# Performance work log

Hardware: AMD Instinct MI355X
Metric: run time of the kernel (lower is better)

## Reference

```python
import jax, jax.numpy as jnp
import numpy as np

D = 512          # model_dim
H = 4 * D        # hidden_mult * model_dim
E = 8            # n_experts
TEMP = 1.0       # temperature
EPS = 1e-5       # torch LayerNorm eps


def setup_inputs() -> dict:
    key = jax.random.key(0)
    ks = jax.random.split(key, 6)
    x = jax.random.normal(ks[0], (4, 4096, D), dtype=jnp.float32)
    # gate: LayerNorm(D) + Linear(D, E)
    gate_gamma = jnp.ones((D,), jnp.float32)
    gate_beta = jnp.zeros((D,), jnp.float32)
    gate_W = jax.random.normal(ks[1], (D, E), jnp.float32) * 0.02
    gate_b = jnp.zeros((E,), jnp.float32)
    # experts stacked along leading E axis: Linear(D,H) -> LeakyReLU -> Linear(H,D)
    W1 = jax.random.normal(ks[2], (E, D, H), jnp.float32) * 0.02
    b1 = jnp.zeros((E, H), jnp.float32)
    W2 = jax.random.normal(ks[3], (E, H, D), jnp.float32) * 0.02
    b2 = jnp.zeros((E, D), jnp.float32)
    return {"x": x, "gate_gamma": gate_gamma, "gate_beta": gate_beta,
            "gate_W": gate_W, "gate_b": gate_b,
            "W1": W1, "b1": b1, "W2": W2, "b2": b2}


def reference(x, gate_gamma, gate_beta, gate_W, gate_b, W1, b1, W2, b2):
    # gate: LayerNorm then Linear, temperature-scaled softmax
    mu = jnp.mean(x, axis=-1, keepdims=True)
    var = jnp.var(x, axis=-1, keepdims=True)  # biased, as in torch LayerNorm
    xn = (x - mu) * jax.lax.rsqrt(var + EPS) * gate_gamma + gate_beta
    logits = (xn @ gate_W + gate_b) / TEMP          # [B,N,E]
    w = jax.nn.softmax(logits, axis=-1)             # [B,N,E]
    # run every expert on all tokens (faithful to soft routing)
    h = jnp.einsum('bnd,edh->benh', x, W1) + b1[None, :, None, :]  # [B,E,N,H]
    h = jax.nn.leaky_relu(h, negative_slope=0.01)
    y = jnp.einsum('benh,ehd->bend', h, W2) + b2[None, :, None, :]  # [B,E,N,D]
    # gate-weighted combine over experts
    out = jnp.einsum('bend,bne->bnd', y, w)
    return out
```

## Files before the change

### kernel.cpp

```cpp
#include <hip/hip_runtime.h>
#include <stdint.h>

#define TD 512
#define TH 2048
#define TE 8
#define TT 16384

typedef __bf16 bf16x8 __attribute__((ext_vector_type(8)));
typedef __bf16 bf16x4 __attribute__((ext_vector_type(4)));
typedef float  f32x4  __attribute__((ext_vector_type(4)));

__device__ __forceinline__ void async16(const void* src, void* lds) {
    __builtin_amdgcn_global_load_lds((const __attribute__((address_space(1))) uint32_t*)src,
                                     (__attribute__((address_space(3))) uint32_t*)lds,
                                     16, 0, 0);
}

__global__ __launch_bounds__(256) void gate_kernel(
    const float* __restrict__ x, const float* __restrict__ gamma,
    const float* __restrict__ beta, const float* __restrict__ gW,
    const float* __restrict__ gb, const float* __restrict__ b2,
    float* __restrict__ gate_w, __bf16* __restrict__ xb,
    float* __restrict__ outp)
{
    const int t    = blockIdx.x * 4 + (threadIdx.x >> 6);
    const int lane = threadIdx.x & 63;

    const float* xr = x + (size_t)t * TD + lane * 8;
    float4 v0 = *(const float4*)xr;
    float4 v1 = *(const float4*)(xr + 4);
    float xv[8] = {v0.x, v0.y, v0.z, v0.w, v1.x, v1.y, v1.z, v1.w};

    float s = 0.f, sq = 0.f;
    #pragma unroll
    for (int j = 0; j < 8; ++j) { s += xv[j]; sq += xv[j] * xv[j]; }
    #pragma unroll
    for (int off = 32; off > 0; off >>= 1) {
        s  += __shfl_xor(s, off);
        sq += __shfl_xor(sq, off);
    }
    const float mean = s * (1.f / TD);
    const float var  = sq * (1.f / TD) - mean * mean;
    const float rs   = rsqrtf(var + 1e-5f);

    bf16x8 xc;
    #pragma unroll
    for (int j = 0; j < 8; ++j) xc[j] = (__bf16)xv[j];
    *(bf16x8*)&xb[(size_t)t * TD + lane * 8] = xc;

    float p[TE] = {};
    #pragma unroll
    for (int j = 0; j < 8; ++j) {
        const int d = lane * 8 + j;
        const float xn = (xv[j] - mean) * rs * gamma[d] + beta[d];
        const float* wr = gW + (size_t)d * TE;
        #pragma unroll
        for (int e = 0; e < TE; ++e) p[e] += xn * wr[e];
    }
    #pragma unroll
    for (int off = 32; off > 0; off >>= 1) {
        #pragma unroll
        for (int e = 0; e < TE; ++e) p[e] += __shfl_xor(p[e], off);
    }

    float m = -3.4e38f;
    #pragma unroll
    for (int e = 0; e < TE; ++e) { p[e] += gb[e]; m = fmaxf(m, p[e]); }
    float sum = 0.f;
    #pragma unroll
    for (int e = 0; e < TE; ++e) { p[e] = expf(p[e] - m); sum += p[e]; }
    const float inv = 1.f / sum;
    if (lane == 0) {
        #pragma unroll
        for (int e = 0; e < TE; ++e) gate_w[(size_t)t * TE + e] = p[e] * inv;
    }

    float ob[8] = {};
    #pragma unroll
    for (int e = 0; e < TE; ++e) {
        const float we = p[e] * inv;
        const float* b2r = b2 + (size_t)e * TD + lane * 8;
        #pragma unroll
        for (int j = 0; j < 8; ++j) ob[j] += we * b2r[j];
    }
    float4 o0 = {ob[0], ob[1], ob[2], ob[3]};
    float4 o1 = {ob[4], ob[5], ob[6], ob[7]};
    *(float4*)&outp[(size_t)t * TD + lane * 8]     = o0;
    *(float4*)&outp[(size_t)t * TD + lane * 8 + 4] = o1;
}

template <int MODE>
__global__ __launch_bounds__(256) void tcast(
    const float* __restrict__ src, __bf16* __restrict__ dst, int R, int C)
{
    __shared__ __bf16 tile[64][65];
    const int e  = blockIdx.z;
    const int r0 = blockIdx.y * 64, c0 = blockIdx.x * 64;
    const int tr = threadIdx.x >> 6;
    const int tc = threadIdx.x & 63;

    const float* s = src + ((size_t)e * R + r0) * C + c0;
    #pragma unroll
    for (int i = 0; i < 16; ++i) {
        const int r = i * 4 + tr;
        tile[r][tc] = (__bf16)s[(size_t)r * C + tc];
    }
    __syncthreads();

    size_t RS, eoff;
    if (MODE == 0) { RS = (size_t)R;     eoff = (size_t)e * C * R; }
    else           { RS = (size_t)2 * R; eoff = (size_t)(e >> 1) * C * 2 * R + (size_t)(e & 1) * R; }

    __bf16* d = dst + eoff + (size_t)c0 * RS + r0;
    #pragma unroll
    for (int i = 0; i < 16; ++i) {
        const int c = i * 4 + tr;
        d[(size_t)c * RS + tc] = tile[tc][c];
    }
}

__global__ __launch_bounds__(256, 2) void gemm1m(
    const __bf16* __restrict__ A, const __bf16* __restrict__ Bt,
    const float* __restrict__ b1, const float* __restrict__ gw,
    __bf16* __restrict__ hC, int grp)
{
    constexpr int S  = TD;
    constexpr int NG = 64;

    __shared__ __align__(16) char smem[49152];

    const int tid  = threadIdx.x;
    const int w    = tid >> 6, lane = tid & 63;
    const int fr   = lane & 15, ks = lane >> 4;

    const int bmg = blockIdx.x & 31;
    const int r   = blockIdx.x >> 5;
    const int bn  = r & 7;
    const int e2  = r >> 3;
    const int e   = grp * 2 + e2;

    const __bf16* Ab  = A  + (size_t)bmg * 512 * S;
    const __bf16* Bb  = Bt + (size_t)e2 * TH * TD + (size_t)bn * 256 * S;
    const float*  b1e = b1 + (size_t)e * TH;

    f32x4 acc[8][4] = {};

    auto stage = [&](int g, int b) {
        const int m4 = g >> 4, kt = g & 15;
        char* aRegion = smem + b * 8192;
        char* bRegion = smem + 16384 + b * 16384;
        const __bf16* Am = Ab + (size_t)m4 * 128 * S;
        #pragma unroll
        for (int p = 0; p < 2; ++p) {
            const int cid = p * 256 + tid;
            const int row = cid >> 2;
            const int gc  = (cid & 3) ^ ((row >> 1) & 3);
            async16(Am + (size_t)row * S + kt * 32 + gc * 8, aRegion + cid * 16);
        }
        #pragma unroll
        for (int p = 0; p < 4; ++p) {
            const int cid = p * 256 + tid;
            const int row = cid >> 2;
            const int gc  = (cid & 3) ^ ((row >> 1) & 3);
            async16(Bb + (size_t)row * S + kt * 32 + gc * 8, bRegion + cid * 16);
        }
    };

    stage(0, 0);
    stage(1, 1);

    for (int g = 0; g < NG; ++g) {
        const int buf = g & 1;
        const char* aR = smem + buf * 8192;
        const char* bR = smem + 16384 + buf * 16384;

        if (g + 1 < NG) { asm volatile("s_waitcnt vmcnt(6)" ::: "memory"); }
        else            { asm volatile("s_waitcnt vmcnt(0)" ::: "memory"); }
        __builtin_amdgcn_sched_barrier(0);
        __builtin_amdgcn_s_barrier();

        bf16x8 areg[8], breg[4];
        #pragma unroll
        for (int m = 0; m < 8; ++m) {
            const int row = m * 16 + fr;
            areg[m] = *(const bf16x8*)(aR + row * 64 + (((ks ^ (row >> 1)) & 3) << 4));
        }
        #pragma unroll
        for (int n = 0; n < 4; ++n) {
            const int row = w * 64 + n * 16 + fr;
            breg[n] = *(const bf16x8*)(bR + row * 64 + (((ks ^ (row >> 1)) & 3) << 4));
        }
        asm volatile("s_waitcnt lgkmcnt(0)" ::: "memory");
        __builtin_amdgcn_sched_barrier(0);
        __builtin_amdgcn_s_barrier();

        if (g + 2 < NG) stage(g + 2, buf);

        __builtin_amdgcn_s_setprio(1);
        #pragma unroll
        for (int m = 0; m < 8; ++m)
            #pragma unroll
            for (int n = 0; n < 4; ++n)
                acc[m][n] = __builtin_amdgcn_mfma_f32_16x16x32_bf16(breg[n], areg[m], acc[m][n], 0, 0, 0);
        __builtin_amdgcn_s_setprio(0);
        __builtin_amdgcn_sched_barrier(0);

        if ((g & 15) == 15) {
            const int m4  = g >> 4;
            const int rjc = (lane >> 4) << 2;
            #pragma unroll
            for (int m = 0; m < 8; ++m) {
                const int row = (bmg * 4 + m4) * 128 + m * 16 + fr;
                const float wgt = gw[(size_t)row * TE + e];
                __bf16* hrow = hC + (size_t)row * (2 * TH) + e2 * TH;
                #pragma unroll
                for (int n = 0; n < 4; ++n) {
                    const int colb = bn * 256 + w * 64 + n * 16 + rjc;
                    const f32x4 bv = *(const f32x4*)&b1e[colb];
                    bf16x4 ov;
                    #pragma unroll
                    for (int j = 0; j < 4; ++j) {
                        float v = acc[m][n][j] + bv[j];
                        v = v > 0.f ? v : 0.01f * v;
                        ov[j] = (__bf16)(v * wgt);
                        acc[m][n][j] = 0.f;
                    }
                    *(bf16x4*)&hrow[colb] = ov;
                }
            }
        }
    }
}

__global__ __launch_bounds__(256, 4) void gemm2f(
    const __bf16* __restrict__ A, const __bf16* __restrict__ Bt,
    float* __restrict__ oC)
{
    constexpr int S  = 2 * TH;
    constexpr int NT = 128;

    __shared__ __align__(16) char smem[32768];

    const int tid  = threadIdx.x;
    const int w    = tid >> 6, lane = tid & 63;
    const int wr   = w >> 1, wc = w & 1;
    const int fr   = lane & 15, ks = lane >> 4;

    const int bm = blockIdx.x & 127;
    const int bn = blockIdx.x >> 7;

    const __bf16* Ab = A  + (size_t)bm * 128 * S;
    const __bf16* Bb = Bt + (size_t)bn * 128 * S;

    f32x4 acc[4][4] = {};

    auto stage = [&](int t, int b) {
        char* aRegion = smem + b * 8192;
        char* bRegion = smem + 16384 + b * 8192;
        #pragma unroll
        for (int p = 0; p < 2; ++p) {
            const int cid = p * 256 + tid;
            const int row = cid >> 2;
            const int gc  = (cid & 3) ^ ((row >> 1) & 3);
            async16(Ab + (size_t)row * S + t * 32 + gc * 8, aRegion + cid * 16);
        }
        #pragma unroll
        for (int p = 0; p < 2; ++p) {
            const int cid = p * 256 + tid;
            const int row = cid >> 2;
            const int gc  = (cid & 3) ^ ((row >> 1) & 3);
            async16(Bb + (size_t)row * S + t * 32 + gc * 8, bRegion + cid * 16);
        }
    };

    stage(0, 0);
    stage(1, 1);

    for (int t = 0; t < NT; ++t) {
        const int buf = t & 1;
        const char* aR = smem + buf * 8192;
        const char* bR = smem + 16384 + buf * 8192;

        if (t + 1 < NT) { asm volatile("s_waitcnt vmcnt(4)" ::: "memory"); }
        else            { asm volatile("s_waitcnt vmcnt(0)" ::: "memory"); }
        __builtin_amdgcn_sched_barrier(0);
        __builtin_amdgcn_s_barrier();

        bf16x8 areg[4], breg[4];
        #pragma unroll
        for (int m = 0; m < 4; ++m) {
            const int row = wr * 64 + m * 16 + fr;
            areg[m] = *(const bf16x8*)(aR + row * 64 + (((ks ^ (row >> 1)) & 3) << 4));
        }
        #pragma unroll
        for (int n = 0; n < 4; ++n) {
            const int row = wc * 64 + n * 16 + fr;
            breg[n] = *(const bf16x8*)(bR + row * 64 + (((ks ^ (row >> 1)) & 3) << 4));
        }
        asm volatile("s_waitcnt lgkmcnt(0)" ::: "memory");
        __builtin_amdgcn_sched_barrier(0);
        __builtin_amdgcn_s_barrier();

        if (t + 2 < NT) stage(t + 2, buf);

        __builtin_amdgcn_s_setprio(1);
        #pragma unroll
        for (int m = 0; m < 4; ++m)
            #pragma unroll
            for (int n = 0; n < 4; ++n)
                acc[m][n] = __builtin_amdgcn_mfma_f32_16x16x32_bf16(areg[m], breg[n], acc[m][n], 0, 0, 0);
        __builtin_amdgcn_s_setprio(0);
        __builtin_amdgcn_sched_barrier(0);
    }

    const int rj = (lane >> 4) << 2;
    #pragma unroll
    for (int m = 0; m < 4; ++m) {
        const int gr0 = bm * 128 + wr * 64 + m * 16 + rj;
        #pragma unroll
        for (int j = 0; j < 4; ++j) {
            const int gr = gr0 + j;
            #pragma unroll
            for (int n = 0; n < 4; ++n) {
                const int gc = bn * 128 + wc * 64 + n * 16 + fr;
                float* op = oC + (size_t)gr * TD + gc;
                *op += acc[m][n][j];
            }
        }
    }
}

extern "C" void kernel_launch(void* const* d_in, const int* in_sizes, int n_in,
                              void* d_out, int out_size, void* d_ws, size_t ws_size,
                              hipStream_t stream)
{
    const float* x     = (const float*)d_in[0];
    const float* gamma = (const float*)d_in[1];
    const float* beta  = (const float*)d_in[2];
    const float* gW    = (const float*)d_in[3];
    const float* gb    = (const float*)d_in[4];
    const float* W1    = (const float*)d_in[5];
    const float* b1    = (const float*)d_in[6];
    const float* W2    = (const float*)d_in[7];
    const float* b2    = (const float*)d_in[8];

    char* ws = (char*)d_ws;
    size_t off = 0;
    float*  gate_w = (float*)(ws + off);  off += (size_t)TT * TE * 4;
    __bf16* xb     = (__bf16*)(ws + off); off += (size_t)TT * TD * 2;
    __bf16* W1t    = (__bf16*)(ws + off); off += (size_t)TE * TD * TH * 2;
    __bf16* W2tc   = (__bf16*)(ws + off); off += (size_t)TE * TD * TH * 2;
    __bf16* h      = (__bf16*)(ws + off);

    gate_kernel<<<TT / 4, 256, 0, stream>>>(x, gamma, beta, gW, gb, b2,
                                            gate_w, xb, (float*)d_out);
    tcast<0><<<dim3(TH / 64, TD / 64, TE), 256, 0, stream>>>(W1, W1t, TD, TH);
    tcast<1><<<dim3(TD / 64, TH / 64, TE), 256, 0, stream>>>(W2, W2tc, TH, TD);

    for (int grp = 0; grp < 4; ++grp) {
        gemm1m<<<512, 256, 0, stream>>>(
            xb, W1t + (size_t)grp * 2 * TH * TD, b1, gate_w, h, grp);
        gemm2f<<<512, 256, 0, stream>>>(
            h, W2tc + (size_t)grp * TD * 2 * TH, (float*)d_out);
    }
}
```

Baseline: 774.4 us.

## Software-pipeline expert GEMMs by fusing GEMM1 of expert c with GEMM2 of c-1

Replaces the four grouped gemm1/gemm2 launch pairs with nine launches of a single fused kernel. Each launch runs GEMM1 for expert c and GEMM2 for expert c-1 concurrently in different blocks, using double-buffered h0/h1 buffers so the two stages overlap and fill the GPU. It also removes the paired-expert W2 layout in favour of per-expert K=2048 GEMM2, and defers the next-stage prefetch until after the epilogue at tile boundaries. The cost is one extra h buffer, GEMM2 blocks running at the 2-blocks-per-CU launch bound instead of 4, and more launches.

```diff
diff --git a/kernel.cpp b/kernel.cpp
--- a/kernel.cpp
+++ b/kernel.cpp
@@ -89,7 +89,6 @@
     *(float4*)&outp[(size_t)t * TD + lane * 8 + 4] = o1;
 }
 
-template <int MODE>
 __global__ __launch_bounds__(256) void tcast(
     const float* __restrict__ src, __bf16* __restrict__ dst, int R, int C)
 {
@@ -107,224 +106,217 @@
     }
     __syncthreads();
 
-    size_t RS, eoff;
-    if (MODE == 0) { RS = (size_t)R;     eoff = (size_t)e * C * R; }
-    else           { RS = (size_t)2 * R; eoff = (size_t)(e >> 1) * C * 2 * R + (size_t)(e & 1) * R; }
-
-    __bf16* d = dst + eoff + (size_t)c0 * RS + r0;
+    __bf16* d = dst + (size_t)e * C * R + (size_t)c0 * R + r0;
     #pragma unroll
     for (int i = 0; i < 16; ++i) {
         const int c = i * 4 + tr;
-        d[(size_t)c * RS + tc] = tile[tc][c];
-    }
-}
-
-__global__ __launch_bounds__(256, 2) void gemm1m(
-    const __bf16* __restrict__ A, const __bf16* __restrict__ Bt,
+        d[(size_t)c * R + tc] = tile[tc][c];
+    }
+}
+
+__global__ __launch_bounds__(256, 2) void moe_fused(
+    const __bf16* __restrict__ xb, const __bf16* __restrict__ W1t,
     const float* __restrict__ b1, const float* __restrict__ gw,
-    __bf16* __restrict__ hC, int grp)
+    __bf16* __restrict__ h0, __bf16* __restrict__ h1,
+    const __bf16* __restrict__ W2t, float* __restrict__ oC,
+    int c, int g1n)
 {
-    constexpr int S  = TD;
-    constexpr int NG = 64;
-
     __shared__ __align__(16) char smem[49152];
 
     const int tid  = threadIdx.x;
     const int w    = tid >> 6, lane = tid & 63;
     const int fr   = lane & 15, ks = lane >> 4;
 
-    const int bmg = blockIdx.x & 31;
-    const int r   = blockIdx.x >> 5;
-    const int bn  = r & 7;
-    const int e2  = r >> 3;
-    const int e   = grp * 2 + e2;
-
-    const __bf16* Ab  = A  + (size_t)bmg * 512 * S;
-    const __bf16* Bb  = Bt + (size_t)e2 * TH * TD + (size_t)bn * 256 * S;
-    const float*  b1e = b1 + (size_t)e * TH;
-
-    f32x4 acc[8][4] = {};
-
-    auto stage = [&](int g, int b) {
-        const int m4 = g >> 4, kt = g & 15;
-        char* aRegion = smem + b * 8192;
-        char* bRegion = smem + 16384 + b * 16384;
-        const __bf16* Am = Ab + (size_t)m4 * 128 * S;
-        #pragma unroll
-        for (int p = 0; p < 2; ++p) {
-            const int cid = p * 256 + tid;
-            const int row = cid >> 2;
-            const int gc  = (cid & 3) ^ ((row >> 1) & 3);
-            async16(Am + (size_t)row * S + kt * 32 + gc * 8, aRegion + cid * 16);
+    if ((int)blockIdx.x < g1n) {
+        const int e = c;
+        __bf16* hD = (c & 1) ? h1 : h0;
+        const __bf16* W1e = W1t + (size_t)e * TH * TD;
+        const float*  b1e = b1 + (size_t)e * TH;
+
+        const int bmg = blockIdx.x & 31;
+        const int bn  = blockIdx.x >> 5;
+        const __bf16* Ab = xb  + (size_t)bmg * 512 * TD;
+        const __bf16* Bb = W1e + (size_t)bn * 256 * TD;
+
+        f32x4 acc[8][4] = {};
+        constexpr int NG = 64;
+
+        auto stage = [&](int g, int b) {
+            const int m4 = g >> 4, kt = g & 15;
+            char* aRegion = smem + b * 8192;
+            char* bRegion = smem + 16384 + b * 16384;
+            const __bf16* Am = Ab + (size_t)m4 * 128 * TD;
+            #pragma unroll
+            for (int p = 0; p < 2; ++p) {
+                const int cid = p * 256 + tid;
+                const int row = cid >> 2;
+                const int gc  = (cid & 3) ^ ((row >> 1) & 3);
+                async16(Am + (size_t)row * TD + kt * 32 + gc * 8, aRegion + cid * 16);
+            }
+            #pragma unroll
+            for (int p = 0; p < 4; ++p) {
+                const int cid = p * 256 + tid;
+                const int row = cid >> 2;
+                const int gc  = (cid & 3) ^ ((row >> 1) & 3);
+                async16(Bb + (size_t)row * TD + kt * 32 + gc * 8, bRegion + cid * 16);
+            }
+        };
+
+        stage(0, 0);
+        stage(1, 1);
+
+        for (int g = 0; g < NG; ++g) {
+            const int buf = g & 1;
+            const char* aR = smem + buf * 8192;
+            const char* bR = smem + 16384 + buf * 16384;
+            const bool bnd = (g & 15) == 15;
+
+            if (g + 1 < NG) { asm volatile("s_waitcnt vmcnt(6)" ::: "memory"); }
+            else            { asm volatile("s_waitcnt vmcnt(0)" ::: "memory"); }
+            __builtin_amdgcn_sched_barrier(0);
+            __builtin_amdgcn_s_barrier();
+
+            bf16x8 areg[8], breg[4];
+            #pragma unroll
+            for (int m = 0; m < 8; ++m) {
+                const int row = m * 16 + fr;
+                areg[m] = *(const bf16x8*)(aR + row * 64 + (((ks ^ (row >> 1)) & 3) << 4));
+            }
+            #pragma unroll
+            for (int n = 0; n < 4; ++n) {
+                const int row = w * 64 + n * 16 + fr;
+                breg[n] = *(const bf16x8*)(bR + row * 64 + (((ks ^ (row >> 1)) & 3) << 4));
+            }
+            asm volatile("s_waitcnt lgkmcnt(0)" ::: "memory");
+            __builtin_amdgcn_sched_barrier(0);
+            __builtin_amdgcn_s_barrier();
+
+            if (!bnd && g + 2 < NG) stage(g + 2, buf);
+
+            __builtin_amdgcn_s_setprio(1);
+            #pragma unroll
+            for (int m = 0; m < 8; ++m)
+                #pragma unroll
+                for (int n = 0; n < 4; ++n)
+                    acc[m][n] = __builtin_amdgcn_mfma_f32_16x16x32_bf16(breg[n], areg[m], acc[m][n], 0, 0, 0);
+            __builtin_amdgcn_s_setprio(0);
+            __builtin_amdgcn_sched_barrier(0);
+
+            if (bnd) {
+                const int m4  = g >> 4;
+                const int rjc = (lane >> 4) << 2;
+                #pragma unroll
+                for (int m = 0; m < 8; ++m) {
+                    const int row = (bmg * 4 + m4) * 128 + m * 16 + fr;
+                    const float wgt = gw[(size_t)row * TE + e];
+                    __bf16* hrow = hD + (size_t)row * TH;
+                    #pragma unroll
+                    for (int n = 0; n < 4; ++n) {
+                        const int colb = bn * 256 + w * 64 + n * 16 + rjc;
+                        const f32x4 bv = *(const f32x4*)&b1e[colb];
+                        bf16x4 ov;
+                        #pragma unroll
+                        for (int j = 0; j < 4; ++j) {
+                            float v = acc[m][n][j] + bv[j];
+                            v = v > 0.f ? v : 0.01f * v;
+                            ov[j] = (__bf16)(v * wgt);
+                            acc[m][n][j] = 0.f;
+                        }
+                        *(bf16x4*)&hrow[colb] = ov;
+                    }
+                }
+                if (g + 2 < NG) stage(g + 2, buf);
+            }
         }
-        #pragma unroll
-        for (int p = 0; p < 4; ++p) {
-            const int cid = p * 256 + tid;
-            const int row = cid >> 2;
-            const int gc  = (cid & 3) ^ ((row >> 1) & 3);
-            async16(Bb + (size_t)row * S + kt * 32 + gc * 8, bRegion + cid * 16);
+    } else {
+        const int e = c - 1;
+        const __bf16* hS  = (e & 1) ? h1 : h0;
+        const __bf16* W2e = W2t + (size_t)e * TD * TH;
+
+        const int bid2 = blockIdx.x - g1n;
+        const int bm   = bid2 & 127;
+        const int bn   = bid2 >> 7;
+        constexpr int S  = TH;
+        constexpr int NT = 64;
+
+        const int wr = w >> 1, wc = w & 1;
+        const __bf16* Ab = hS  + (size_t)bm * 128 * S;
+        const __bf16* Bb = W2e + (size_t)bn * 128 * S;
+
+        f32x4 acc[4][4] = {};
+
+        auto stage = [&](int t, int b) {
+            char* aRegion = smem + b * 8192;
+            char* bRegion = smem + 16384 + b * 8192;
+            #pragma unroll
+            for (int p = 0; p < 2; ++p) {
+                const int cid = p * 256 + tid;
+                const int row = cid >> 2;
+                const int gc  = (cid & 3) ^ ((row >> 1) & 3);
+                async16(Ab + (size_t)row * S + t * 32 + gc * 8, aRegion + cid * 16);
+            }
+            #pragma unroll
+            for (int p = 0; p < 2; ++p) {
+                const int cid = p * 256 + tid;
+                const int row = cid >> 2;
+                const int gc  = (cid & 3) ^ ((row >> 1) & 3);
+                async16(Bb + (size_t)row * S + t * 32 + gc * 8, bRegion + cid * 16);
+            }
+        };
+
+        stage(0, 0);
+        stage(1, 1);
+
+        for (int t = 0; t < NT; ++t) {
+            const int buf = t & 1;
+            const char* aR = smem + buf * 8192;
+            const char* bR = smem + 16384 + buf * 8192;
+
+            if (t + 1 < NT) { asm volatile("s_waitcnt vmcnt(4)" ::: "memory"); }
+            else            { asm volatile("s_waitcnt vmcnt(0)" ::: "memory"); }
+            __builtin_amdgcn_sched_barrier(0);
+            __builtin_amdgcn_s_barrier();
+
+            bf16x8 areg[4], breg[4];
+            #pragma unroll
+            for (int m = 0; m < 4; ++m) {
+                const int row = wr * 64 + m * 16 + fr;
+                areg[m] = *(const bf16x8*)(aR + row * 64 + (((ks ^ (row >> 1)) & 3) << 4));
+            }
+            #pragma unroll
+            for (int n = 0; n < 4; ++n) {
+                const int row = wc * 64 + n * 16 + fr;
+                breg[n] = *(const bf16x8*)(bR + row * 64 + (((ks ^ (row >> 1)) & 3) << 4));
+            }
+            asm volatile("s_waitcnt lgkmcnt(0)" ::: "memory");
+            __builtin_amdgcn_sched_barrier(0);
+            __builtin_amdgcn_s_barrier();
+
+            if (t + 2 < NT) stage(t + 2, buf);
+
+            __builtin_amdgcn_s_setprio(1);
+            #pragma unroll
+            for (int m = 0; m < 4; ++m)
+                #pragma unroll
+                for (int n = 0; n < 4; ++n)
+                    acc[m][n] = __builtin_amdgcn_mfma_f32_16x16x32_bf16(areg[m], breg[n], acc[m][n], 0, 0, 0);
+            __builtin_amdgcn_s_setprio(0);
+            __builtin_amdgcn_sched_barrier(0);
         }
-    };
-
-    stage(0, 0);
-    stage(1, 1);
-
-    for (int g = 0; g < NG; ++g) {
-        const int buf = g & 1;
-        const char* aR = smem + buf * 8192;
-        const char* bR = smem + 16384 + buf * 16384;
-
-        if (g + 1 < NG) { asm volatile("s_waitcnt vmcnt(6)" ::: "memory"); }
-        else            { asm volatile("s_waitcnt vmcnt(0)" ::: "memory"); }
-        __builtin_amdgcn_sched_barrier(0);
-        __builtin_amdgcn_s_barrier();
-
-        bf16x8 areg[8], breg[4];
-        #pragma unroll
-        for (int m = 0; m < 8; ++m) {
-            const int row = m * 16 + fr;
-            areg[m] = *(const bf16x8*)(aR + row * 64 + (((ks ^ (row >> 1)) & 3) << 4));
-        }
-        #pragma unroll
-        for (int n = 0; n < 4; ++n) {
-            const int row = w * 64 + n * 16 + fr;
-            breg[n] = *(const bf16x8*)(bR + row * 64 + (((ks ^ (row >> 1)) & 3) << 4));
-        }
-        asm volatile("s_waitcnt lgkmcnt(0)" ::: "memory");
-        __builtin_amdgcn_sched_barrier(0);
-        __builtin_amdgcn_s_barrier();
-
-        if (g + 2 < NG) stage(g + 2, buf);
-
-        __builtin_amdgcn_s_setprio(1);
-        #pragma unroll
-        for (int m = 0; m < 8; ++m)
-            #pragma unroll
-            for (int n = 0; n < 4; ++n)
-                acc[m][n] = __builtin_amdgcn_mfma_f32_16x16x32_bf16(breg[n], areg[m], acc[m][n], 0, 0, 0);
-        __builtin_amdgcn_s_setprio(0);
-        __builtin_amdgcn_sched_barrier(0);
-
-        if ((g & 15) == 15) {
-            const int m4  = g >> 4;
-            const int rjc = (lane >> 4) << 2;
-            #pragma unroll
-            for (int m = 0; m < 8; ++m) {
-                const int row = (bmg * 4 + m4) * 128 + m * 16 + fr;
-                const float wgt = gw[(size_t)row * TE + e];
-                __bf16* hrow = hC + (size_t)row * (2 * TH) + e2 * TH;
+
+        const int rj = (lane >> 4) << 2;
+        #pragma unroll
+        for (int m = 0; m < 4; ++m) {
+            const int gr0 = bm * 128 + wr * 64 + m * 16 + rj;
+            #pragma unroll
+            for (int j = 0; j < 4; ++j) {
+                const int gr = gr0 + j;
                 #pragma unroll
                 for (int n = 0; n < 4; ++n) {
-                    const int colb = bn * 256 + w * 64 + n * 16 + rjc;
-                    const f32x4 bv = *(const f32x4*)&b1e[colb];
-                    bf16x4 ov;
-                    #pragma unroll
-                    for (int j = 0; j < 4; ++j) {
-                        float v = acc[m][n][j] + bv[j];
-                        v = v > 0.f ? v : 0.01f * v;
-                        ov[j] = (__bf16)(v * wgt);
-                        acc[m][n][j] = 0.f;
-                    }
-                    *(bf16x4*)&hrow[colb] = ov;
+                    const int gc = bn * 128 + wc * 64 + n * 16 + fr;
+                    float* op = oC + (size_t)gr * TD + gc;
+                    *op += acc[m][n][j];
                 }
-            }
-        }
-    }
-}
-
-__global__ __launch_bounds__(256, 4) void gemm2f(
-    const __bf16* __restrict__ A, const __bf16* __restrict__ Bt,
-    float* __restrict__ oC)
-{
-    constexpr int S  = 2 * TH;
-    constexpr int NT = 128;
-
-    __shared__ __align__(16) char smem[32768];
-
-    const int tid  = threadIdx.x;
-    const int w    = tid >> 6, lane = tid & 63;
-    const int wr   = w >> 1, wc = w & 1;
-    const int fr   = lane & 15, ks = lane >> 4;
-
-    const int bm = blockIdx.x & 127;
-    const int bn = blockIdx.x >> 7;
-
-    const __bf16* Ab = A  + (size_t)bm * 128 * S;
-    const __bf16* Bb = Bt + (size_t)bn * 128 * S;
-
-    f32x4 acc[4][4] = {};
-
-    auto stage = [&](int t, int b) {
-        char* aRegion = smem + b * 8192;
-        char* bRegion = smem + 16384 + b * 8192;
-        #pragma unroll
-        for (int p = 0; p < 2; ++p) {
-            const int cid = p * 256 + tid;
-            const int row = cid >> 2;
-            const int gc  = (cid & 3) ^ ((row >> 1) & 3);
-            async16(Ab + (size_t)row * S + t * 32 + gc * 8, aRegion + cid * 16);
-        }
-        #pragma unroll
-        for (int p = 0; p < 2; ++p) {
-            const int cid = p * 256 + tid;
-            const int row = cid >> 2;
-            const int gc  = (cid & 3) ^ ((row >> 1) & 3);
-            async16(Bb + (size_t)row * S + t * 32 + gc * 8, bRegion + cid * 16);
-        }
-    };
-
-    stage(0, 0);
-    stage(1, 1);
-
-    for (int t = 0; t < NT; ++t) {
-        const int buf = t & 1;
-        const char* aR = smem + buf * 8192;
-        const char* bR = smem + 16384 + buf * 8192;
-
-        if (t + 1 < NT) { asm volatile("s_waitcnt vmcnt(4)" ::: "memory"); }
-        else            { asm volatile("s_waitcnt vmcnt(0)" ::: "memory"); }
-        __builtin_amdgcn_sched_barrier(0);
-        __builtin_amdgcn_s_barrier();
-
-        bf16x8 areg[4], breg[4];
-        #pragma unroll
-        for (int m = 0; m < 4; ++m) {
-            const int row = wr * 64 + m * 16 + fr;
-            areg[m] = *(const bf16x8*)(aR + row * 64 + (((ks ^ (row >> 1)) & 3) << 4));
-        }
-        #pragma unroll
-        for (int n = 0; n < 4; ++n) {
-            const int row = wc * 64 + n * 16 + fr;
-            breg[n] = *(const bf16x8*)(bR + row * 64 + (((ks ^ (row >> 1)) & 3) << 4));
-        }
-        asm volatile("s_waitcnt lgkmcnt(0)" ::: "memory");
-        __builtin_amdgcn_sched_barrier(0);
-        __builtin_amdgcn_s_barrier();
-
-        if (t + 2 < NT) stage(t + 2, buf);
-
-        __builtin_amdgcn_s_setprio(1);
-        #pragma unroll
-        for (int m = 0; m < 4; ++m)
-            #pragma unroll
-            for (int n = 0; n < 4; ++n)
-                acc[m][n] = __builtin_amdgcn_mfma_f32_16x16x32_bf16(areg[m], breg[n], acc[m][n], 0, 0, 0);
-        __builtin_amdgcn_s_setprio(0);
-        __builtin_amdgcn_sched_barrier(0);
-    }
-
-    const int rj = (lane >> 4) << 2;
-    #pragma unroll
-    for (int m = 0; m < 4; ++m) {
-        const int gr0 = bm * 128 + wr * 64 + m * 16 + rj;
-        #pragma unroll
-        for (int j = 0; j < 4; ++j) {
-            const int gr = gr0 + j;
-            #pragma unroll
-            for (int n = 0; n < 4; ++n) {
-                const int gc = bn * 128 + wc * 64 + n * 16 + fr;
-                float* op = oC + (size_t)gr * TD + gc;
-                *op += acc[m][n][j];
             }
         }
     }
@@ -349,18 +341,19 @@
     float*  gate_w = (float*)(ws + off);  off += (size_t)TT * TE * 4;
     __bf16* xb     = (__bf16*)(ws + off); off += (size_t)TT * TD * 2;
     __bf16* W1t    = (__bf16*)(ws + off); off += (size_t)TE * TD * TH * 2;
-    __bf16* W2tc   = (__bf16*)(ws + off); off += (size_t)TE * TD * TH * 2;
-    __bf16* h      = (__bf16*)(ws + off);
+    __bf16* W2t    = (__bf16*)(ws + off); off += (size_t)TE * TD * TH * 2;
+    __bf16* h0     = (__bf16*)(ws + off); off += (size_t)TT * TH * 2;
+    __bf16* h1     = (__bf16*)(ws + off);
 
     gate_kernel<<<TT / 4, 256, 0, stream>>>(x, gamma, beta, gW, gb, b2,
                                             gate_w, xb, (float*)d_out);
-    tcast<0><<<dim3(TH / 64, TD / 64, TE), 256, 0, stream>>>(W1, W1t, TD, TH);
-    tcast<1><<<dim3(TD / 64, TH / 64, TE), 256, 0, stream>>>(W2, W2tc, TH, TD);
-
-    for (int grp = 0; grp < 4; ++grp) {
-        gemm1m<<<512, 256, 0, stream>>>(
-            xb, W1t + (size_t)grp * 2 * TH * TD, b1, gate_w, h, grp);
-        gemm2f<<<512, 256, 0, stream>>>(
-            h, W2tc + (size_t)grp * TD * 2 * TH, (float*)d_out);
-    }
-}
+    tcast<<<dim3(TH / 64, TD / 64, TE), 256, 0, stream>>>(W1, W1t, TD, TH);
+    tcast<<<dim3(TD / 64, TH / 64, TE), 256, 0, stream>>>(W2, W2t, TH, TD);
+
+    for (int c = 0; c <= TE; ++c) {
+        const int g1n  = (c < TE) ? 256 : 0;
+        const int g2n  = (c > 0) ? 512 : 0;
+        moe_fused<<<g1n + g2n, 256, 0, stream>>>(
+            xb, W1t, b1, gate_w, h0, h1, W2t, (float*)d_out, c, g1n);
+    }
+}
```

New measurement: 841.0 us. 8.6% more time.
